# Optimization experiments

Hardware: AMD Instinct MI355X
Metric: run time of the kernel (lower is better)

The kernel has to match this reference:

```python
import jax, jax.numpy as jnp
import numpy as np

N_NODES = 50000
N_EDGES = 600000
HIDDEN = 128
HEADS = 8
OUT_CH = HIDDEN // HEADS
NUM_LAYERS = 3
NEG_SLOPE = 0.2   # PyG GATConv default leaky_relu slope
BN_EPS = 1e-5

# Note: dropout is a no-op in eval mode; BatchNorm uses batch statistics
# (training-mode math, the only well-defined choice without running stats).

def setup_inputs() -> dict:
    key = jax.random.key(0)
    ks = jax.random.split(key, 9)
    x = jax.random.normal(ks[0], (N_NODES, HIDDEN), dtype=jnp.float32)
    edge_index = jax.random.randint(ks[1], (2, N_EDGES), 0, N_NODES, dtype=jnp.int64)
    s = 1.0 / np.sqrt(HIDDEN)
    W = jax.random.normal(ks[2], (NUM_LAYERS, HIDDEN, HEADS * OUT_CH), dtype=jnp.float32) * s
    att_src = jax.random.normal(ks[3], (NUM_LAYERS, HEADS, OUT_CH), dtype=jnp.float32) * s
    att_dst = jax.random.normal(ks[4], (NUM_LAYERS, HEADS, OUT_CH), dtype=jnp.float32) * s
    bias = jnp.zeros((NUM_LAYERS, HIDDEN), dtype=jnp.float32)
    gamma = jnp.ones((NUM_LAYERS, HIDDEN), dtype=jnp.float32)
    beta = jnp.zeros((NUM_LAYERS, HIDDEN), dtype=jnp.float32)
    return {"x": x, "edge_index": edge_index, "W": W, "att_src": att_src,
            "att_dst": att_dst, "bias": bias, "gamma": gamma, "beta": beta}


def _gat_layer(x, src, dst, W, a_src, a_dst, b):
    n = x.shape[0]
    h = (x @ W).reshape(n, HEADS, OUT_CH)              # [N,H,C]
    alpha_s = jnp.einsum('nhc,hc->nh', h, a_src)        # [N,H]
    alpha_d = jnp.einsum('nhc,hc->nh', h, a_dst)
    e = jax.nn.leaky_relu(alpha_s[src] + alpha_d[dst], NEG_SLOPE)  # [E,H]
    # segment softmax over incoming edges of each destination node
    m = jax.ops.segment_max(e, dst, num_segments=n)     # [N,H]
    e = jnp.exp(e - m[dst])
    z = jax.ops.segment_sum(e, dst, num_segments=n)
    alpha = e / (z[dst] + 1e-16)                        # [E,H]
    msg = h[src] * alpha[:, :, None]                    # [E,H,C]
    out = jax.ops.segment_sum(msg, dst, num_segments=n) # [N,H,C]
    return out.reshape(n, HEADS * OUT_CH) + b


def _batchnorm(x, gamma, beta):
    mu = x.mean(axis=0)
    var = x.var(axis=0)
    return (x - mu) * jax.lax.rsqrt(var + BN_EPS) * gamma + beta


def reference(x, edge_index, W, att_src, att_dst, bias, gamma, beta):
    src, dst = edge_index[0], edge_index[1]
    for l in range(NUM_LAYERS):
        x = _gat_layer(x, src, dst, W[l], att_src[l], att_dst[l], bias[l])
        x = _batchnorm(x, gamma[l], beta[l])
        x = jax.nn.elu(x)
    return x
```

## Files before the change

kernel.cpp:

```cpp
#include <hip/hip_runtime.h>
#include <hip/hip_bf16.h>

#define N_NODES 50000
#define N_EDGES 600000
#define HID 128
#define HEADS 8
#define OUTC 16
#define NEG_SLOPE 0.2f
#define BN_EPS 1e-5f

typedef __attribute__((ext_vector_type(8))) short short8;
typedef __attribute__((ext_vector_type(4))) float floatx4;

__device__ __forceinline__ float bf_lo(unsigned int v) { return __uint_as_float(v << 16); }
__device__ __forceinline__ float bf_hi(unsigned int v) { return __uint_as_float(v & 0xffff0000u); }

__device__ __forceinline__ short f2bfs(float v) {
    __hip_bfloat16 b = __float2bfloat16(v);
    return *reinterpret_cast<short*>(&b);
}

__global__ void k_hist_prep(const int* __restrict__ dst, int* __restrict__ deg, int e, int nb_e,
                            const float* __restrict__ W, const float* __restrict__ asrc,
                            const float* __restrict__ adst,
                            __hip_bfloat16* __restrict__ Wt, __hip_bfloat16* __restrict__ WAT) {
    if ((int)blockIdx.x < nb_e) {
        int i = blockIdx.x * 256 + threadIdx.x;
        if (i < e) atomicAdd(&deg[dst[i]], 1);
        return;
    }
    int i = (blockIdx.x - nb_e) * 256 + threadIdx.x;
    if (i < 3 * 16384) {
        int l = i >> 14, r = i & 16383, n = r >> 7, k = r & 127;
        Wt[i] = __float2bfloat16(W[l * 16384 + k * 128 + n]);
    } else {
        int j2 = i - 3 * 16384;
        if (j2 < 3 * 2048) {
            int l = j2 >> 11, r = j2 & 2047, j = r >> 7, k = r & 127;
            const float* att = (j < 8) ? (asrc + l * 128 + j * 16) : (adst + l * 128 + (j - 8) * 16);
            const float* Wrow = W + l * 16384 + k * 128 + (j & 7) * 16;
            float sum = 0.f;
#pragma unroll
            for (int c = 0; c < 16; c++) sum += Wrow[c] * att[c];
            WAT[j2] = __float2bfloat16(sum);
        }
    }
}

__global__ void k_scan1(const int* __restrict__ deg, int* __restrict__ incl,
                        int* __restrict__ partials, int n) {
    __shared__ int sh[512];
    int i = blockIdx.x * 512 + threadIdx.x;
    int v = (i < n) ? deg[i] : 0;
    sh[threadIdx.x] = v;
    __syncthreads();
    for (int off = 1; off < 512; off <<= 1) {
        int t = (threadIdx.x >= off) ? sh[threadIdx.x - off] : 0;
        __syncthreads();
        sh[threadIdx.x] += t;
        __syncthreads();
    }
    if (i < n) incl[i] = sh[threadIdx.x];
    if (threadIdx.x == 511) partials[blockIdx.x] = sh[511];
}

__global__ void k_scan23(const int* __restrict__ deg, const int* __restrict__ incl,
                         const int* __restrict__ partials, int* __restrict__ row_ptr,
                         int* __restrict__ cursor, int n, int e_total, int nb) {
    __shared__ int sp[128];
    int t = threadIdx.x;
    int orig = 0;
    if (t < 128) {
        orig = (t < nb) ? partials[t] : 0;
        sp[t] = orig;
    }
    __syncthreads();
    for (int off = 1; off < 128; off <<= 1) {
        int v = (t < 128 && t >= off) ? sp[t - off] : 0;
        __syncthreads();
        if (t < 128) sp[t] += v;
        __syncthreads();
    }
    if (t < 128) sp[t] -= orig;
    __syncthreads();
    int i = blockIdx.x * 512 + t;
    if (i < n) {
        int rp = incl[i] - deg[i] + sp[blockIdx.x];
        row_ptr[i] = rp;
        cursor[i] = rp;
    }
    if (i == 0) row_ptr[n] = e_total;
}

__global__ void k_scatter(const int* __restrict__ src, const int* __restrict__ dst,
                          int* __restrict__ cursor, int* __restrict__ col_src, int e) {
    int i = blockIdx.x * 256 + threadIdx.x;
    if (i < e) {
        int d = dst[i];
        int p = atomicAdd(&cursor[d], 1);
        col_src[p] = src[i];
    }
}

__global__ __launch_bounds__(256) void k_gemm(const float* __restrict__ Xf,
                                              const float* __restrict__ stats,
                                              const float* __restrict__ gamma,
                                              const float* __restrict__ beta,
                                              const __hip_bfloat16* __restrict__ Wt,
                                              const __hip_bfloat16* __restrict__ WAT,
                                              __hip_bfloat16* __restrict__ Hb,
                                              float* __restrict__ AS, float* __restrict__ AD,
                                              int n_nodes, int apply_bn) {
    __shared__ float s_scale[128], s_shift[128];
    if (apply_bn && threadIdx.x < 128) {
        int c = threadIdx.x;
        float invN = 1.0f / (float)N_NODES;
        float mu = stats[c] * invN;
        float var = stats[128 + c] * invN - mu * mu;
        float sc = rsqrtf(var + BN_EPS) * gamma[c];
        s_scale[c] = sc;
        s_shift[c] = beta[c] - mu * sc;
    }
    __syncthreads();

    int wave = threadIdx.x >> 6, lane = threadIdx.x & 63;
    int row0 = blockIdx.x * 64 + wave * 16;
    int m_lane = lane & 15, kq = lane >> 4;
    floatx4 acc[8] = {};
    floatx4 acc_a = {};
    const short* Ws = (const short*)Wt;
    const short* Was = (const short*)WAT;
    int r = row0 + m_lane;
    int rr = (r < n_nodes) ? r : 0;
    for (int c = 0; c < 4; c++) {
        const float4* xp = (const float4*)(Xf + (size_t)rr * 128 + c * 32 + kq * 8);
        float4 v0 = xp[0], v1 = xp[1];
        float vals[8] = {v0.x, v0.y, v0.z, v0.w, v1.x, v1.y, v1.z, v1.w};
        short8 a;
        if (apply_bn) {
            int ch0 = c * 32 + kq * 8;
#pragma unroll
            for (int j = 0; j < 8; j++) {
                float val = fmaf(vals[j], s_scale[ch0 + j], s_shift[ch0 + j]);
                val = (val > 0.f) ? val : (__expf(val) - 1.0f);
                a[j] = f2bfs(val);
            }
        } else {
#pragma unroll
            for (int j = 0; j < 8; j++)
                a[j] = f2bfs(vals[j]);
        }
        for (int t = 0; t < 8; t++) {
            short8 b = *(const short8*)(Ws + (t * 16 + m_lane) * 128 + c * 32 + kq * 8);
            acc[t] = __builtin_amdgcn_mfma_f32_16x16x32_bf16(a, b, acc[t], 0, 0, 0);
        }
        short8 bwa = *(const short8*)(Was + m_lane * 128 + c * 32 + kq * 8);
        acc_a = __builtin_amdgcn_mfma_f32_16x16x32_bf16(a, bwa, acc_a, 0, 0, 0);
    }
#pragma unroll
    for (int reg = 0; reg < 4; reg++) {
        int row = row0 + kq * 4 + reg;
        if (row >= n_nodes) continue;
#pragma unroll
        for (int t = 0; t < 8; t++)
            Hb[(size_t)row * 128 + t * 16 + m_lane] = __float2bfloat16(acc[t][reg]);
        float av = acc_a[reg];
        if (m_lane < 8) AS[row * 8 + m_lane] = av;
        else            AD[row * 8 + (m_lane - 8)] = av;
    }
}

__global__ __launch_bounds__(256) void k_agg(const int* __restrict__ RP,
                                             const int* __restrict__ COL,
                                             const float* __restrict__ AS,
                                             const float* __restrict__ AD,
                                             const __hip_bfloat16* __restrict__ Hb,
                                             const float* __restrict__ bias,
                                             float* __restrict__ out,
                                             float* __restrict__ par2, int n_nodes) {
    __shared__ float s_sum[4][128];
    __shared__ float s_sq[4][128];
    int wave = threadIdx.x >> 6, lane = threadIdx.x & 63;
    int n = blockIdx.x * 4 + wave;
    bool valid = (n < n_nodes);
    int e_l = lane >> 4, q = lane & 15, h = q >> 1;
    s_sum[wave][lane] = 0.f; s_sum[wave][lane + 64] = 0.f;
    s_sq[wave][lane] = 0.f;  s_sq[wave][lane + 64] = 0.f;

    int p0 = valid ? RP[n] : 0;
    int p1 = valid ? RP[n + 1] : 0;
    float ad = valid ? AD[n * 8 + h] : 0.f;
    float z = 0.f;
    float acc[8];
#pragma unroll
    for (int c = 0; c < 8; c++) acc[c] = 0.f;
    const unsigned short* Hu = (const unsigned short*)Hb;
    for (int p = p0 + e_l; p < p1; p += 4) {
        int s = COL[p];
        float e = AS[s * 8 + h] + ad;
        e = (e > 0.f) ? e : NEG_SLOPE * e;
        float w = __expf(e);
        z += w;
        const uint4 hv = *(const uint4*)(Hu + (size_t)s * 128 + q * 8);
        acc[0] += w * bf_lo(hv.x); acc[1] += w * bf_hi(hv.x);
        acc[2] += w * bf_lo(hv.y); acc[3] += w * bf_hi(hv.y);
        acc[4] += w * bf_lo(hv.z); acc[5] += w * bf_hi(hv.z);
        acc[6] += w * bf_lo(hv.w); acc[7] += w * bf_hi(hv.w);
    }
#pragma unroll
    for (int off = 16; off < 64; off <<= 1) {
        z += __shfl_xor(z, off, 64);
#pragma unroll
        for (int c = 0; c < 8; c++) acc[c] += __shfl_xor(acc[c], off, 64);
    }
    if (valid && e_l == 0) {
        float inv = 1.0f / (z + 1e-16f);
        const float* bp = bias + q * 8;
        float v[8];
#pragma unroll
        for (int c = 0; c < 8; c++) v[c] = fmaf(acc[c], inv, bp[c]);
        float4* op = (float4*)(out + (size_t)n * 128 + q * 8);
        op[0] = make_float4(v[0], v[1], v[2], v[3]);
        op[1] = make_float4(v[4], v[5], v[6], v[7]);
        int ch0 = q * 8;
#pragma unroll
        for (int c = 0; c < 8; c++) {
            s_sum[wave][ch0 + c] = v[c];
            s_sq[wave][ch0 + c] = v[c] * v[c];
        }
    }
    __syncthreads();
    int tid = threadIdx.x;
    float tot;
    if (tid < 128) {
        tot = s_sum[0][tid] + s_sum[1][tid] + s_sum[2][tid] + s_sum[3][tid];
    } else {
        int cc = tid - 128;
        tot = s_sq[0][cc] + s_sq[1][cc] + s_sq[2][cc] + s_sq[3][cc];
    }
    atomicAdd(&par2[(blockIdx.x & 63) * 256 + tid], tot);
}

__global__ void k_bnreduce(float* __restrict__ par2, float* __restrict__ stats) {
    int t = threadIdx.x;
    float s = 0.f;
#pragma unroll 8
    for (int b = 0; b < 64; b++) s += par2[b * 256 + t];
    stats[t] = s;
#pragma unroll 8
    for (int b = 0; b < 64; b++) par2[b * 256 + t] = 0.f;
}

__global__ void k_bnapply(const float* __restrict__ x, const float* __restrict__ stats,
                          const float* __restrict__ gamma, const float* __restrict__ beta,
                          float* __restrict__ outf, int n_nodes) {
    int i = blockIdx.x * 256 + threadIdx.x;
    if (i >= n_nodes * 32) return;
    float4 v = *(const float4*)(x + (size_t)i * 4);
    int c0 = (i * 4) & 127;
    float r[4] = {v.x, v.y, v.z, v.w};
    float invN = 1.0f / (float)N_NODES;
#pragma unroll
    for (int j = 0; j < 4; j++) {
        int c = c0 + j;
        float mu = stats[c] * invN;
        float var = stats[128 + c] * invN - mu * mu;
        float sc = rsqrtf(var + BN_EPS) * gamma[c];
        float val = (r[j] - mu) * sc + beta[c];
        val = (val > 0.f) ? val : (__expf(val) - 1.0f);
        r[j] = val;
    }
    *(float4*)(outf + (size_t)i * 4) = make_float4(r[0], r[1], r[2], r[3]);
}

extern "C" void kernel_launch(void* const* d_in, const int* in_sizes, int n_in,
                              void* d_out, int out_size, void* d_ws, size_t ws_size,
                              hipStream_t stream) {
    const float* x_in   = (const float*)d_in[0];
    const int*   eidx   = (const int*)d_in[1];
    const float* W      = (const float*)d_in[2];
    const float* attsrc = (const float*)d_in[3];
    const float* attdst = (const float*)d_in[4];
    const float* bias   = (const float*)d_in[5];
    const float* gamma  = (const float*)d_in[6];
    const float* beta   = (const float*)d_in[7];
    float* out = (float*)d_out;

    const int N = N_NODES, E = N_EDGES;
    const int* src = eidx;
    const int* dst = eidx + E;

    char* base = (char*)d_ws;
    size_t off = 0;
    auto carve = [&](size_t bytes) -> char* {
        char* p = base + off;
        off += (bytes + 255) & ~(size_t)255;
        return p;
    };
    __hip_bfloat16* Hb  = (__hip_bfloat16*)carve((size_t)N * HID * 2);
    float*          XN  = (float*)carve((size_t)N * HID * 4);
    float*          AS  = (float*)carve((size_t)N * HEADS * 4);
    float*          AD  = (float*)carve((size_t)N * HEADS * 4);
    __hip_bfloat16* WT  = (__hip_bfloat16*)carve((size_t)3 * HID * HID * 2);
    __hip_bfloat16* WAT = (__hip_bfloat16*)carve((size_t)3 * 16 * HID * 2);
    float*          STA = (float*)carve(3 * 256 * 4);
    int*            DEG = (int*)carve((size_t)N * 4);
    float*          PAR2 = (float*)carve(64 * 256 * 4);
    int*            INC = (int*)carve((size_t)N * 4);
    int*            RP  = (int*)carve((size_t)(N + 1) * 4);
    int*            CUR = (int*)carve((size_t)N * 4);
    int*            PRT = (int*)carve(1024 * 4);
    int*            COL = (int*)carve((size_t)E * 4);

    const int NB_E  = (E + 255) / 256;
    const int NB_SC = (N + 511) / 512;
    const int PREP_B = (3 * 16384 + 3 * 2048 + 255) / 256;

    size_t zlen = (size_t)((char*)(PAR2 + 64 * 256) - (char*)DEG);
    (void)hipMemsetAsync(DEG, 0, zlen, stream);

    k_hist_prep<<<NB_E + PREP_B, 256, 0, stream>>>(dst, DEG, E, NB_E, W, attsrc, attdst, WT, WAT);
    k_scan1<<<NB_SC, 512, 0, stream>>>(DEG, INC, PRT, N);
    k_scan23<<<NB_SC, 512, 0, stream>>>(DEG, INC, PRT, RP, CUR, N, E, NB_SC);
    k_scatter<<<NB_E, 256, 0, stream>>>(src, dst, CUR, COL, E);

    for (int l = 0; l < 3; l++) {
        const float* Xf = (l == 0) ? x_in : XN;
        const float* st = (l == 0) ? nullptr : (STA + (l - 1) * 256);
        const float* gm = gamma + (l - 1) * 128;
        const float* bt = beta + (l - 1) * 128;
        k_gemm<<<(N + 63) / 64, 256, 0, stream>>>(Xf, st, gm, bt,
                                                  WT + l * 16384, WAT + l * 2048,
                                                  Hb, AS, AD, N, (l == 0) ? 0 : 1);
        k_agg<<<(N + 3) / 4, 256, 0, stream>>>(RP, COL, AS, AD, Hb, bias + l * 128,
                                               XN, PAR2, N);
        k_bnreduce<<<1, 256, 0, stream>>>(PAR2, STA + l * 256);
    }
    k_bnapply<<<(N * 32 + 255) / 256, 256, 0, stream>>>(XN, STA + 2 * 256,
                                                        gamma + 2 * 128, beta + 2 * 128, out, N);
}
```

Measured before the change: 363.7 us.

## Precompute per-edge attention weights in separate kernel and unroll aggregation loop

Adds a per-edge kernel that computes the leaky-relu/exp attention weights for all 8 heads using a stored destination index per CSR slot. The aggregation kernel then reads these precomputed weights instead of gathering AS and computing exp per edge, and processes two edges per iteration to raise memory-level parallelism. This trades the redundant per-lane exp and AS gathers for an extra launch per layer and roughly 19MB of extra write-then-read traffic for the weight buffer, plus a row-index array built during scatter.

Result: slower. 386.2 us (+6.2%).

```diff
diff --git a/kernel.cpp b/kernel.cpp
--- a/kernel.cpp
+++ b/kernel.cpp
@@ -93,12 +93,14 @@
 }
 
 __global__ void k_scatter(const int* __restrict__ src, const int* __restrict__ dst,
-                          int* __restrict__ cursor, int* __restrict__ col_src, int e) {
+                          int* __restrict__ cursor, int* __restrict__ col_src,
+                          int* __restrict__ row_dst, int e) {
     int i = blockIdx.x * 256 + threadIdx.x;
     if (i < e) {
         int d = dst[i];
         int p = atomicAdd(&cursor[d], 1);
         col_src[p] = src[i];
+        row_dst[p] = d;
     }
 }
 
@@ -170,10 +172,34 @@
     }
 }
 
+__global__ __launch_bounds__(256) void k_edgew(const int* __restrict__ COL,
+                                               const int* __restrict__ ROW,
+                                               const float* __restrict__ AS,
+                                               const float* __restrict__ AD,
+                                               float* __restrict__ WE, int e) {
+    int p = blockIdx.x * 256 + threadIdx.x;
+    if (p >= e) return;
+    int s = COL[p], d = ROW[p];
+    const float4* asp = (const float4*)(AS + (size_t)s * 8);
+    const float4* adp = (const float4*)(AD + (size_t)d * 8);
+    float4 a0 = asp[0], a1 = asp[1];
+    float4 b0 = adp[0], b1 = adp[1];
+    float ev[8] = {a0.x + b0.x, a0.y + b0.y, a0.z + b0.z, a0.w + b0.w,
+                   a1.x + b1.x, a1.y + b1.y, a1.z + b1.z, a1.w + b1.w};
+#pragma unroll
+    for (int j = 0; j < 8; j++) {
+        float t = ev[j];
+        t = (t > 0.f) ? t : NEG_SLOPE * t;
+        ev[j] = __expf(t);
+    }
+    float4* wp = (float4*)(WE + (size_t)p * 8);
+    wp[0] = make_float4(ev[0], ev[1], ev[2], ev[3]);
+    wp[1] = make_float4(ev[4], ev[5], ev[6], ev[7]);
+}
+
 __global__ __launch_bounds__(256) void k_agg(const int* __restrict__ RP,
                                              const int* __restrict__ COL,
-                                             const float* __restrict__ AS,
-                                             const float* __restrict__ AD,
+                                             const float* __restrict__ WE,
                                              const __hip_bfloat16* __restrict__ Hb,
                                              const float* __restrict__ bias,
                                              float* __restrict__ out,
@@ -189,23 +215,38 @@
 
     int p0 = valid ? RP[n] : 0;
     int p1 = valid ? RP[n + 1] : 0;
-    float ad = valid ? AD[n * 8 + h] : 0.f;
     float z = 0.f;
     float acc[8];
 #pragma unroll
     for (int c = 0; c < 8; c++) acc[c] = 0.f;
     const unsigned short* Hu = (const unsigned short*)Hb;
-    for (int p = p0 + e_l; p < p1; p += 4) {
-        int s = COL[p];
-        float e = AS[s * 8 + h] + ad;
-        e = (e > 0.f) ? e : NEG_SLOPE * e;
-        float w = __expf(e);
-        z += w;
-        const uint4 hv = *(const uint4*)(Hu + (size_t)s * 128 + q * 8);
-        acc[0] += w * bf_lo(hv.x); acc[1] += w * bf_hi(hv.x);
-        acc[2] += w * bf_lo(hv.y); acc[3] += w * bf_hi(hv.y);
-        acc[4] += w * bf_lo(hv.z); acc[5] += w * bf_hi(hv.z);
-        acc[6] += w * bf_lo(hv.w); acc[7] += w * bf_hi(hv.w);
+    int p = p0 + e_l;
+    for (; p + 4 < p1; p += 8) {
+        int s0 = COL[p];
+        int s1 = COL[p + 4];
+        float w0 = WE[(size_t)p * 8 + h];
+        float w1 = WE[(size_t)(p + 4) * 8 + h];
+        const uint4 hv0 = *(const uint4*)(Hu + (size_t)s0 * 128 + q * 8);
+        const uint4 hv1 = *(const uint4*)(Hu + (size_t)s1 * 128 + q * 8);
+        z += w0 + w1;
+        acc[0] += w0 * bf_lo(hv0.x); acc[1] += w0 * bf_hi(hv0.x);
+        acc[2] += w0 * bf_lo(hv0.y); acc[3] += w0 * bf_hi(hv0.y);
+        acc[4] += w0 * bf_lo(hv0.z); acc[5] += w0 * bf_hi(hv0.z);
+        acc[6] += w0 * bf_lo(hv0.w); acc[7] += w0 * bf_hi(hv0.w);
+        acc[0] += w1 * bf_lo(hv1.x); acc[1] += w1 * bf_hi(hv1.x);
+        acc[2] += w1 * bf_lo(hv1.y); acc[3] += w1 * bf_hi(hv1.y);
+        acc[4] += w1 * bf_lo(hv1.z); acc[5] += w1 * bf_hi(hv1.z);
+        acc[6] += w1 * bf_lo(hv1.w); acc[7] += w1 * bf_hi(hv1.w);
+    }
+    if (p < p1) {
+        int s0 = COL[p];
+        float w0 = WE[(size_t)p * 8 + h];
+        const uint4 hv0 = *(const uint4*)(Hu + (size_t)s0 * 128 + q * 8);
+        z += w0;
+        acc[0] += w0 * bf_lo(hv0.x); acc[1] += w0 * bf_hi(hv0.x);
+        acc[2] += w0 * bf_lo(hv0.y); acc[3] += w0 * bf_hi(hv0.y);
+        acc[4] += w0 * bf_lo(hv0.z); acc[5] += w0 * bf_hi(hv0.z);
+        acc[6] += w0 * bf_lo(hv0.w); acc[7] += w0 * bf_hi(hv0.w);
     }
 #pragma unroll
     for (int off = 16; off < 64; off <<= 1) {
@@ -311,6 +352,8 @@
     int*            CUR = (int*)carve((size_t)N * 4);
     int*            PRT = (int*)carve(1024 * 4);
     int*            COL = (int*)carve((size_t)E * 4);
+    int*            ROW = (int*)carve((size_t)E * 4);
+    float*          WE  = (float*)carve((size_t)E * HEADS * 4);
 
     const int NB_E  = (E + 255) / 256;
     const int NB_SC = (N + 511) / 512;
@@ -322,7 +365,7 @@
     k_hist_prep<<<NB_E + PREP_B, 256, 0, stream>>>(dst, DEG, E, NB_E, W, attsrc, attdst, WT, WAT);
     k_scan1<<<NB_SC, 512, 0, stream>>>(DEG, INC, PRT, N);
     k_scan23<<<NB_SC, 512, 0, stream>>>(DEG, INC, PRT, RP, CUR, N, E, NB_SC);
-    k_scatter<<<NB_E, 256, 0, stream>>>(src, dst, CUR, COL, E);
+    k_scatter<<<NB_E, 256, 0, stream>>>(src, dst, CUR, COL, ROW, E);
 
     for (int l = 0; l < 3; l++) {
         const float* Xf = (l == 0) ? x_in : XN;
@@ -332,7 +375,8 @@
         k_gemm<<<(N + 63) / 64, 256, 0, stream>>>(Xf, st, gm, bt,
                                                   WT + l * 16384, WAT + l * 2048,
                                                   Hb, AS, AD, N, (l == 0) ? 0 : 1);
-        k_agg<<<(N + 3) / 4, 256, 0, stream>>>(RP, COL, AS, AD, Hb, bias + l * 128,
+        k_edgew<<<NB_E, 256, 0, stream>>>(COL, ROW, AS, AD, WE, E);
+        k_agg<<<(N + 3) / 4, 256, 0, stream>>>(RP, COL, WE, Hb, bias + l * 128,
                                                XN, PAR2, N);
         k_bnreduce<<<1, 256, 0, stream>>>(PAR2, STA + l * 256);
     }
```
